# Optimization experiments

Measured on AMD Instinct MI355X. Metric: run time of the kernel, lower is better.

## Reference

```python
import jax, jax.numpy as jnp
from jax import lax
import numpy as np

MAXLEN, B, D = 2048, 64, 256
CONV_CH = 512

def setup_inputs() -> dict:
    key = jax.random.key(0)
    ks = jax.random.split(key, 10)
    inp = {
        "ctx_val": jax.random.normal(ks[0], (MAXLEN, B, D), jnp.float32),
        "ctx_key": jax.random.normal(ks[1], (MAXLEN, B, D), jnp.float32),
        "ctx_mask": jnp.ones((MAXLEN, B), jnp.float32),
        "attention_past": jax.random.uniform(ks[2], (B, 1, MAXLEN), jnp.float32),
        "ht_query": jax.random.normal(ks[3], (B, D), jnp.float32),
        # learned parameters (torch default inits approximated with scaled normals)
        "W_conv": jax.random.normal(ks[4], (CONV_CH, 1, 3), jnp.float32) * (1.0 / np.sqrt(3.0)),
        "W_query": jax.random.normal(ks[5], (D, D), jnp.float32) * (1.0 / np.sqrt(D)),
        "W_att_past": jax.random.normal(ks[6], (D, CONV_CH), jnp.float32) * (1.0 / np.sqrt(CONV_CH)),
        "b_att_past": jax.random.normal(ks[7], (D,), jnp.float32) * 0.01,
        "W_attn": jax.random.normal(ks[8], (1, D), jnp.float32) * (1.0 / np.sqrt(D)),
        "b_attn": jax.random.normal(ks[9], (1,), jnp.float32) * 0.01,
    }
    return inp

def reference(ctx_val, ctx_key, ctx_mask, attention_past, ht_query,
              W_conv, W_query, W_att_past, b_att_past, W_attn, b_attn):
    # fc_query: (b, D)
    hq = ht_query @ W_query.T
    # conv1d(1->512, k=3, pad=1, no bias): (b, 512, L)
    ap = lax.conv_general_dilated(attention_past, W_conv, window_strides=(1,),
                                  padding=[(1, 1)],
                                  dimension_numbers=("NCH", "OIH", "NCH"))
    # permute(2,0,1) -> (L, b, 512), then fc_att_past -> (L, b, D)
    ap = jnp.einsum("blc,dc->lbd", jnp.transpose(ap, (2, 0, 1)).transpose(1, 0, 2), W_att_past) + b_att_past
    # additive attention score: (L, b)
    s = jnp.tanh(ctx_key + hq[None, :, :] + ap)
    score = jnp.einsum("lbd,d->lb", s, W_attn[0]) + b_attn[0]
    # hard threshold mask, normalize over seq dim
    hard = (score >= 0).astype(jnp.float32) * ctx_mask
    hard = hard / (hard.sum(axis=0) + 1e-10)
    # masked weighted sum over seq dim: (b, D)
    ct = jnp.einsum("lbd,lb->bd", ctx_val, hard)
    return (ct, hard)
```

## Files before the change

kernel.cpp:

```cpp
#include <hip/hip_runtime.h>
#include <math.h>

#define L_MAX 2048
#define BATCH 64
#define DIM   256
#define CCH   512
#define ROWSTRIDE (BATCH * DIM)

#define HQ_OFF   0
#define WF_OFF   16384
#define SUMS_OFF 17152
#define HARD_OFF 19200
#define PART_OFF 150272
#define SUMS_STRIDE 32

__device__ __forceinline__ float fast_tanh(float x) {
    float ax = fabsf(x);
    float e  = __expf(2.0f * ax);
    float r  = 1.0f - 2.0f * __builtin_amdgcn_rcpf(e + 1.0f);
    return copysignf(r, x);
}

__global__ __launch_bounds__(256) void prep_kernel(
    const float* __restrict__ ht_query, const float* __restrict__ W_query,
    const float* __restrict__ W_conv,   const float* __restrict__ W_att_past,
    float* __restrict__ hq, float* __restrict__ wf, float* __restrict__ sums) {
    int t   = threadIdx.x;
    int blk = blockIdx.x;
    if (blk == 0 && t < BATCH) sums[t * SUMS_STRIDE] = 0.f;
    __shared__ float q[DIM];
    if (blk < BATCH) {
        q[t] = ht_query[blk * DIM + t];
        __syncthreads();
        const float4* wrow = (const float4*)(W_query + t * DIM);
        float acc = 0.f;
        #pragma unroll 8
        for (int k = 0; k < DIM / 4; k++) {
            float4 wv = wrow[k];
            acc += q[4*k] * wv.x + q[4*k+1] * wv.y + q[4*k+2] * wv.z + q[4*k+3] * wv.w;
        }
        hq[blk * DIM + t] = acc;
    } else {
        int j = blk - BATCH;
        const float4* wrow = (const float4*)(W_att_past + t * CCH);
        float acc = 0.f;
        #pragma unroll 8
        for (int c = 0; c < CCH / 4; c++) {
            float4 wv = wrow[c];
            acc += W_conv[(4*c  ) * 3 + j] * wv.x + W_conv[(4*c+1) * 3 + j] * wv.y
                 + W_conv[(4*c+2) * 3 + j] * wv.z + W_conv[(4*c+3) * 3 + j] * wv.w;
        }
        wf[j * DIM + t] = acc;
    }
}

__global__ __launch_bounds__(256) void fused_kernel(
    const float* __restrict__ ctx_key, const float* __restrict__ ctx_val,
    const float* __restrict__ ctx_mask, const float* __restrict__ att_past,
    const float* __restrict__ hq, const float* __restrict__ wf,
    const float* __restrict__ b_att_past, const float* __restrict__ W_attn,
    const float* __restrict__ b_attn,
    float* __restrict__ hard_raw, float* __restrict__ sums,
    float* __restrict__ part) {
    int b     = blockIdx.x & 63;
    int chunk = blockIdx.x >> 6;
    int w     = threadIdx.x >> 6;
    int lane  = threadIdx.x & 63;
    int d0    = lane << 2;
    int l0    = chunk * 64 + w * 16;

    float4 hq4 = *(const float4*)(hq + b * DIM + d0);
    float4 bp  = *(const float4*)(b_att_past + d0);
    hq4.x += bp.x; hq4.y += bp.y; hq4.z += bp.z; hq4.w += bp.w;
    float4 w0  = *(const float4*)(wf + d0);
    float4 w1  = *(const float4*)(wf + DIM + d0);
    float4 w2  = *(const float4*)(wf + 2 * DIM + d0);
    float4 wa  = *(const float4*)(W_attn + d0);
    float battn = b_attn[0];
    const float* apb = att_past + b * L_MAX;

    float ap[18];
    {
        float4 t0 = *(const float4*)(apb + l0);
        float4 t1 = *(const float4*)(apb + l0 + 4);
        float4 t2 = *(const float4*)(apb + l0 + 8);
        float4 t3 = *(const float4*)(apb + l0 + 12);
        ap[1]=t0.x; ap[2]=t0.y; ap[3]=t0.z; ap[4]=t0.w;
        ap[5]=t1.x; ap[6]=t1.y; ap[7]=t1.z; ap[8]=t1.w;
        ap[9]=t2.x; ap[10]=t2.y; ap[11]=t2.z; ap[12]=t2.w;
        ap[13]=t3.x; ap[14]=t3.y; ap[15]=t3.z; ap[16]=t3.w;
        ap[0]  = (l0 > 0)          ? apb[l0 - 1]  : 0.f;
        ap[17] = (l0 + 16 < L_MAX) ? apb[l0 + 16] : 0.f;
    }

    const float* key_base = ctx_key + (size_t)(l0 * BATCH + b) * DIM + d0;
    const float* val_base = ctx_val + (size_t)(l0 * BATCH + b) * DIM + d0;

    float4 k16[16];
    float m16[16];
    #pragma unroll
    for (int j = 0; j < 16; j++)
        k16[j] = *(const float4*)(key_base + (size_t)j * ROWSTRIDE);
    #pragma unroll
    for (int j = 0; j < 16; j++)
        m16[j] = ctx_mask[(l0 + j) * BATCH + b];

    float p[16];
    #pragma unroll
    for (int j = 0; j < 16; j++) {
        float am = ap[j], a0 = ap[j + 1], a1 = ap[j + 2];
        float x0 = k16[j].x + hq4.x + am * w0.x + a0 * w1.x + a1 * w2.x;
        float x1 = k16[j].y + hq4.y + am * w0.y + a0 * w1.y + a1 * w2.y;
        float x2 = k16[j].z + hq4.z + am * w0.z + a0 * w1.z + a1 * w2.z;
        float x3 = k16[j].w + hq4.w + am * w0.w + a0 * w1.w + a1 * w2.w;
        p[j] = fast_tanh(x0) * wa.x + fast_tanh(x1) * wa.y +
               fast_tanh(x2) * wa.z + fast_tanh(x3) * wa.w;
    }
    #pragma unroll
    for (int off = 32; off > 0; off >>= 1) {
        #pragma unroll
        for (int j = 0; j < 16; j++)
            p[j] += __shfl_xor(p[j], off, 64);
    }

    float h[16];
    float cnt = 0.f;
    #pragma unroll
    for (int j = 0; j < 16; j++) {
        h[j] = (p[j] + battn >= 0.f) ? m16[j] : 0.f;
        cnt += h[j];
    }
    if (lane == 0) {
        #pragma unroll
        for (int j = 0; j < 16; j++)
            hard_raw[(l0 + j) * BATCH + b] = h[j];
    }

    float4 acc = make_float4(0.f, 0.f, 0.f, 0.f);
    float4 v16[16];
    #pragma unroll
    for (int j = 0; j < 16; j++) {
        size_t off = (h[j] != 0.f) ? (size_t)j * ROWSTRIDE : 0;
        v16[j] = *(const float4*)(val_base + off);
    }
    #pragma unroll
    for (int j = 0; j < 16; j++) {
        acc.x += v16[j].x * h[j]; acc.y += v16[j].y * h[j];
        acc.z += v16[j].z * h[j]; acc.w += v16[j].w * h[j];
    }

    __shared__ float red[4 * DIM];
    *(float4*)(red + w * DIM + d0) = acc;
    __shared__ float c4[4];
    if (lane == 0) c4[w] = cnt;
    __syncthreads();
    int d = threadIdx.x;
    float s = red[d] + red[DIM + d] + red[2 * DIM + d] + red[3 * DIM + d];
    part[(size_t)(chunk * BATCH + b) * DIM + d] = s;
    if (threadIdx.x == 0)
        atomicAdd(&sums[b * SUMS_STRIDE], c4[0] + c4[1] + c4[2] + c4[3]);
}

__global__ __launch_bounds__(256) void tail_kernel(
    const float* __restrict__ part, const float* __restrict__ hard_raw,
    const float* __restrict__ sums,
    float* __restrict__ ct, float* __restrict__ out_hard) {
    if (blockIdx.x < BATCH) {
        int b = blockIdx.x;
        int d = threadIdx.x;
        float s = 0.f;
        #pragma unroll 8
        for (int c = 0; c < 32; c++)
            s += part[(size_t)(c * BATCH + b) * DIM + d];
        float invZ = 1.0f / (sums[b * SUMS_STRIDE] + 1e-10f);
        ct[b * DIM + d] = s * invZ;
    } else {
        int i = (blockIdx.x - BATCH) * 256 + threadIdx.x;
        float4 h = *(const float4*)(hard_raw + (size_t)i * 4);
        int b0 = (i * 4) & 63;
        float4 o;
        o.x = h.x / (sums[(b0 + 0) * SUMS_STRIDE] + 1e-10f);
        o.y = h.y / (sums[(b0 + 1) * SUMS_STRIDE] + 1e-10f);
        o.z = h.z / (sums[(b0 + 2) * SUMS_STRIDE] + 1e-10f);
        o.w = h.w / (sums[(b0 + 3) * SUMS_STRIDE] + 1e-10f);
        *(float4*)(out_hard + (size_t)i * 4) = o;
    }
}

extern "C" void kernel_launch(void* const* d_in, const int* in_sizes, int n_in,
                              void* d_out, int out_size, void* d_ws, size_t ws_size,
                              hipStream_t stream) {
    const float* ctx_val    = (const float*)d_in[0];
    const float* ctx_key    = (const float*)d_in[1];
    const float* ctx_mask   = (const float*)d_in[2];
    const float* att_past   = (const float*)d_in[3];
    const float* ht_query   = (const float*)d_in[4];
    const float* W_conv     = (const float*)d_in[5];
    const float* W_query    = (const float*)d_in[6];
    const float* W_att_past = (const float*)d_in[7];
    const float* b_att_past = (const float*)d_in[8];
    const float* W_attn     = (const float*)d_in[9];
    const float* b_attn     = (const float*)d_in[10];

    float* ws   = (float*)d_ws;
    float* hq   = ws + HQ_OFF;
    float* wf   = ws + WF_OFF;
    float* sums = ws + SUMS_OFF;
    float* hard = ws + HARD_OFF;
    float* part = ws + PART_OFF;

    float* out_ct   = (float*)d_out;
    float* out_hard = (float*)d_out + BATCH * DIM;

    prep_kernel<<<BATCH + 3, 256, 0, stream>>>(
        ht_query, W_query, W_conv, W_att_past, hq, wf, sums);

    fused_kernel<<<BATCH * 32, 256, 0, stream>>>(
        ctx_key, ctx_val, ctx_mask, att_past, hq, wf, b_att_past, W_attn, b_attn,
        hard, sums, part);

    tail_kernel<<<BATCH + 128, 256, 0, stream>>>(part, hard, sums, out_ct, out_hard);
}
```

Before: 324.2 us.

## Split sequence into more chunks per block and replace atomic count sums with per-chunk counts

Each block now covers 16 sequence positions instead of 64, so the fused kernel launches four times as many blocks (8192) and each thread keeps only 4 key/value rows in registers. This is meant to raise occupancy and memory-level parallelism for the bandwidth-bound streaming of ctx_key and ctx_val. The atomicAdd into per-batch sums is replaced by per-chunk count writes that the tail kernel reduces. In exchange the partial-sum buffer grows fourfold and the tail kernel does more reduction work.

```diff
diff --git a/kernel.cpp b/kernel.cpp
--- a/kernel.cpp
+++ b/kernel.cpp
@@ -6,13 +6,13 @@
 #define DIM   256
 #define CCH   512
 #define ROWSTRIDE (BATCH * DIM)
+#define NCHUNK 128
 
 #define HQ_OFF   0
 #define WF_OFF   16384
-#define SUMS_OFF 17152
-#define HARD_OFF 19200
-#define PART_OFF 150272
-#define SUMS_STRIDE 32
+#define HARD_OFF 17152
+#define PART_OFF 148224
+#define CNTS_OFF 2245376
 
 __device__ __forceinline__ float fast_tanh(float x) {
     float ax = fabsf(x);
@@ -24,10 +24,9 @@
 __global__ __launch_bounds__(256) void prep_kernel(
     const float* __restrict__ ht_query, const float* __restrict__ W_query,
     const float* __restrict__ W_conv,   const float* __restrict__ W_att_past,
-    float* __restrict__ hq, float* __restrict__ wf, float* __restrict__ sums) {
+    float* __restrict__ hq, float* __restrict__ wf) {
     int t   = threadIdx.x;
     int blk = blockIdx.x;
-    if (blk == 0 && t < BATCH) sums[t * SUMS_STRIDE] = 0.f;
     __shared__ float q[DIM];
     if (blk < BATCH) {
         q[t] = ht_query[blk * DIM + t];
@@ -60,14 +59,14 @@
     const float* __restrict__ hq, const float* __restrict__ wf,
     const float* __restrict__ b_att_past, const float* __restrict__ W_attn,
     const float* __restrict__ b_attn,
-    float* __restrict__ hard_raw, float* __restrict__ sums,
+    float* __restrict__ hard_raw, float* __restrict__ cnts,
     float* __restrict__ part) {
     int b     = blockIdx.x & 63;
     int chunk = blockIdx.x >> 6;
     int w     = threadIdx.x >> 6;
     int lane  = threadIdx.x & 63;
     int d0    = lane << 2;
-    int l0    = chunk * 64 + w * 16;
+    int l0    = chunk * 16 + w * 4;
 
     float4 hq4 = *(const float4*)(hq + b * DIM + d0);
     float4 bp  = *(const float4*)(b_att_past + d0);
@@ -79,110 +78,115 @@
     float battn = b_attn[0];
     const float* apb = att_past + b * L_MAX;
 
-    float ap[18];
+    float ap[6];
     {
         float4 t0 = *(const float4*)(apb + l0);
-        float4 t1 = *(const float4*)(apb + l0 + 4);
-        float4 t2 = *(const float4*)(apb + l0 + 8);
-        float4 t3 = *(const float4*)(apb + l0 + 12);
-        ap[1]=t0.x; ap[2]=t0.y; ap[3]=t0.z; ap[4]=t0.w;
-        ap[5]=t1.x; ap[6]=t1.y; ap[7]=t1.z; ap[8]=t1.w;
-        ap[9]=t2.x; ap[10]=t2.y; ap[11]=t2.z; ap[12]=t2.w;
-        ap[13]=t3.x; ap[14]=t3.y; ap[15]=t3.z; ap[16]=t3.w;
-        ap[0]  = (l0 > 0)          ? apb[l0 - 1]  : 0.f;
-        ap[17] = (l0 + 16 < L_MAX) ? apb[l0 + 16] : 0.f;
+        ap[1] = t0.x; ap[2] = t0.y; ap[3] = t0.z; ap[4] = t0.w;
+        ap[0] = (l0 > 0)         ? apb[l0 - 1] : 0.f;
+        ap[5] = (l0 + 4 < L_MAX) ? apb[l0 + 4] : 0.f;
     }
 
     const float* key_base = ctx_key + (size_t)(l0 * BATCH + b) * DIM + d0;
     const float* val_base = ctx_val + (size_t)(l0 * BATCH + b) * DIM + d0;
 
-    float4 k16[16];
-    float m16[16];
-    #pragma unroll
-    for (int j = 0; j < 16; j++)
-        k16[j] = *(const float4*)(key_base + (size_t)j * ROWSTRIDE);
-    #pragma unroll
-    for (int j = 0; j < 16; j++)
-        m16[j] = ctx_mask[(l0 + j) * BATCH + b];
-
-    float p[16];
-    #pragma unroll
-    for (int j = 0; j < 16; j++) {
+    float4 k4[4];
+    float m4[4];
+    #pragma unroll
+    for (int j = 0; j < 4; j++)
+        k4[j] = *(const float4*)(key_base + (size_t)j * ROWSTRIDE);
+    #pragma unroll
+    for (int j = 0; j < 4; j++)
+        m4[j] = ctx_mask[(l0 + j) * BATCH + b];
+
+    float p[4];
+    #pragma unroll
+    for (int j = 0; j < 4; j++) {
         float am = ap[j], a0 = ap[j + 1], a1 = ap[j + 2];
-        float x0 = k16[j].x + hq4.x + am * w0.x + a0 * w1.x + a1 * w2.x;
-        float x1 = k16[j].y + hq4.y + am * w0.y + a0 * w1.y + a1 * w2.y;
-        float x2 = k16[j].z + hq4.z + am * w0.z + a0 * w1.z + a1 * w2.z;
-        float x3 = k16[j].w + hq4.w + am * w0.w + a0 * w1.w + a1 * w2.w;
+        float x0 = k4[j].x + hq4.x + am * w0.x + a0 * w1.x + a1 * w2.x;
+        float x1 = k4[j].y + hq4.y + am * w0.y + a0 * w1.y + a1 * w2.y;
+        float x2 = k4[j].z + hq4.z + am * w0.z + a0 * w1.z + a1 * w2.z;
+        float x3 = k4[j].w + hq4.w + am * w0.w + a0 * w1.w + a1 * w2.w;
         p[j] = fast_tanh(x0) * wa.x + fast_tanh(x1) * wa.y +
                fast_tanh(x2) * wa.z + fast_tanh(x3) * wa.w;
     }
     #pragma unroll
     for (int off = 32; off > 0; off >>= 1) {
         #pragma unroll
-        for (int j = 0; j < 16; j++)
+        for (int j = 0; j < 4; j++)
             p[j] += __shfl_xor(p[j], off, 64);
     }
 
-    float h[16];
+    float h[4];
     float cnt = 0.f;
     #pragma unroll
-    for (int j = 0; j < 16; j++) {
-        h[j] = (p[j] + battn >= 0.f) ? m16[j] : 0.f;
+    for (int j = 0; j < 4; j++) {
+        h[j] = (p[j] + battn >= 0.f) ? m4[j] : 0.f;
         cnt += h[j];
     }
     if (lane == 0) {
         #pragma unroll
-        for (int j = 0; j < 16; j++)
+        for (int j = 0; j < 4; j++)
             hard_raw[(l0 + j) * BATCH + b] = h[j];
     }
 
+    float4 v4[4];
+    #pragma unroll
+    for (int j = 0; j < 4; j++) {
+        size_t off = (h[j] != 0.f) ? (size_t)j * ROWSTRIDE : 0;
+        v4[j] = *(const float4*)(val_base + off);
+    }
     float4 acc = make_float4(0.f, 0.f, 0.f, 0.f);
-    float4 v16[16];
-    #pragma unroll
-    for (int j = 0; j < 16; j++) {
-        size_t off = (h[j] != 0.f) ? (size_t)j * ROWSTRIDE : 0;
-        v16[j] = *(const float4*)(val_base + off);
-    }
-    #pragma unroll
-    for (int j = 0; j < 16; j++) {
-        acc.x += v16[j].x * h[j]; acc.y += v16[j].y * h[j];
-        acc.z += v16[j].z * h[j]; acc.w += v16[j].w * h[j];
+    #pragma unroll
+    for (int j = 0; j < 4; j++) {
+        acc.x += v4[j].x * h[j]; acc.y += v4[j].y * h[j];
+        acc.z += v4[j].z * h[j]; acc.w += v4[j].w * h[j];
     }
 
     __shared__ float red[4 * DIM];
+    __shared__ float c4[4];
     *(float4*)(red + w * DIM + d0) = acc;
-    __shared__ float c4[4];
     if (lane == 0) c4[w] = cnt;
     __syncthreads();
     int d = threadIdx.x;
     float s = red[d] + red[DIM + d] + red[2 * DIM + d] + red[3 * DIM + d];
     part[(size_t)(chunk * BATCH + b) * DIM + d] = s;
     if (threadIdx.x == 0)
-        atomicAdd(&sums[b * SUMS_STRIDE], c4[0] + c4[1] + c4[2] + c4[3]);
+        cnts[chunk * BATCH + b] = c4[0] + c4[1] + c4[2] + c4[3];
 }
 
 __global__ __launch_bounds__(256) void tail_kernel(
     const float* __restrict__ part, const float* __restrict__ hard_raw,
-    const float* __restrict__ sums,
+    const float* __restrict__ cnts,
     float* __restrict__ ct, float* __restrict__ out_hard) {
     if (blockIdx.x < BATCH) {
         int b = blockIdx.x;
         int d = threadIdx.x;
+        float z = 0.f;
+        #pragma unroll 8
+        for (int c = 0; c < NCHUNK; c++) z += cnts[c * BATCH + b];
         float s = 0.f;
         #pragma unroll 8
-        for (int c = 0; c < 32; c++)
+        for (int c = 0; c < NCHUNK; c++)
             s += part[(size_t)(c * BATCH + b) * DIM + d];
-        float invZ = 1.0f / (sums[b * SUMS_STRIDE] + 1e-10f);
-        ct[b * DIM + d] = s * invZ;
+        ct[b * DIM + d] = s / (z + 1e-10f);
     } else {
-        int i = (blockIdx.x - BATCH) * 256 + threadIdx.x;
+        __shared__ float zs[BATCH];
+        int t = threadIdx.x;
+        if (t < BATCH) {
+            float z = 0.f;
+            #pragma unroll 8
+            for (int c = 0; c < NCHUNK; c++) z += cnts[c * BATCH + t];
+            zs[t] = z;
+        }
+        __syncthreads();
+        int i = (blockIdx.x - BATCH) * 256 + t;
         float4 h = *(const float4*)(hard_raw + (size_t)i * 4);
         int b0 = (i * 4) & 63;
         float4 o;
-        o.x = h.x / (sums[(b0 + 0) * SUMS_STRIDE] + 1e-10f);
-        o.y = h.y / (sums[(b0 + 1) * SUMS_STRIDE] + 1e-10f);
-        o.z = h.z / (sums[(b0 + 2) * SUMS_STRIDE] + 1e-10f);
-        o.w = h.w / (sums[(b0 + 3) * SUMS_STRIDE] + 1e-10f);
+        o.x = h.x / (zs[b0 + 0] + 1e-10f);
+        o.y = h.y / (zs[b0 + 1] + 1e-10f);
+        o.z = h.z / (zs[b0 + 2] + 1e-10f);
+        o.w = h.w / (zs[b0 + 3] + 1e-10f);
         *(float4*)(out_hard + (size_t)i * 4) = o;
     }
 }
@@ -205,19 +209,19 @@
     float* ws   = (float*)d_ws;
     float* hq   = ws + HQ_OFF;
     float* wf   = ws + WF_OFF;
-    float* sums = ws + SUMS_OFF;
     float* hard = ws + HARD_OFF;
     float* part = ws + PART_OFF;
+    float* cnts = ws + CNTS_OFF;
 
     float* out_ct   = (float*)d_out;
     float* out_hard = (float*)d_out + BATCH * DIM;
 
     prep_kernel<<<BATCH + 3, 256, 0, stream>>>(
-        ht_query, W_query, W_conv, W_att_past, hq, wf, sums);
-
-    fused_kernel<<<BATCH * 32, 256, 0, stream>>>(
+        ht_query, W_query, W_conv, W_att_past, hq, wf);
+
+    fused_kernel<<<BATCH * NCHUNK, 256, 0, stream>>>(
         ctx_key, ctx_val, ctx_mask, att_past, hq, wf, b_att_past, W_attn, b_attn,
-        hard, sums, part);
-
-    tail_kernel<<<BATCH + 128, 256, 0, stream>>>(part, hard, sums, out_ct, out_hard);
-}
+        hard, cnts, part);
+
+    tail_kernel<<<BATCH + 128, 256, 0, stream>>>(part, hard, cnts, out_ct, out_hard);
+}
```

New measurement: 326.0 us. About the same (+0.5%).
